# Optimization experiments

Hardware: AMD Instinct MI355X
Metric: run time of the kernel (lower is better)

Reference implementation:

```python
import jax, jax.numpy as jnp
import numpy as np

CUTOFF = 5.0
N_PER_L = (20, 18, 16, 14)   # radial features per angular channel l (max_radial=20, Laplacian-eigenstate style taper)
M_PER_L = (1, 3, 5, 7)       # 2l+1
N_ATOMS = 10000
N_EDGES = 200000
N_SPECIES = 100
PSEUDO = 4

_FREQS = np.concatenate([np.arange(1, nl + 1) for nl in N_PER_L]).astype(np.float32)  # [sum(N_PER_L)]


def _radial(r):
    # r: [P] -> [P, sum(N_PER_L)]. Sine (spherical Laplacian eigenstate style) basis with smooth cosine cutoff.
    rc = jnp.clip(r, 0.0, CUTOFF)
    fc = 0.5 * (jnp.cos(jnp.pi * rc / CUTOFF) + 1.0)            # [P]
    return jnp.sin(jnp.asarray(_FREQS) * (jnp.pi / CUTOFF) * r[:, None]) * fc[:, None]


def _angular(R, r):
    # real spherical harmonics up to l=3, [P, 16], ordered l-major (m = -l..l)
    u = R / (r[:, None] + 1e-12)
    x, y, z = u[:, 0], u[:, 1], u[:, 2]
    x2, y2, z2 = x * x, y * y, z * z
    cols = [
        jnp.full_like(x, 0.28209479177387814),
        0.4886025119029199 * y, 0.4886025119029199 * z, 0.4886025119029199 * x,
        1.0925484305920792 * x * y, 1.0925484305920792 * y * z,
        0.31539156525252005 * (3.0 * z2 - 1.0),
        1.0925484305920792 * x * z, 0.5462742152960396 * (x2 - y2),
        0.5900435899266435 * y * (3.0 * x2 - y2), 2.890611442640554 * x * y * z,
        0.4570457994644658 * y * (5.0 * z2 - 1.0), 0.3731763325901154 * z * (5.0 * z2 - 3.0),
        0.4570457994644658 * x * (5.0 * z2 - 1.0), 1.445305721320277 * z * (x2 - y2),
        0.5900435899266435 * x * (x2 - 3.0 * y2),
    ]
    return jnp.stack(cols, axis=-1)


def setup_inputs() -> dict:
    key = jax.random.key(0)
    k1, k2, k3, k4, k5 = jax.random.split(key, 5)
    return {
        "R_ij": jax.random.normal(k1, (N_EDGES, 3), dtype=jnp.float32) * 1.5,
        "i": jnp.sort(jax.random.randint(k2, (N_EDGES,), 0, N_ATOMS)),
        "j": jax.random.randint(k3, (N_EDGES,), 0, N_ATOMS),
        "species": jax.random.randint(k4, (N_ATOMS,), 0, N_SPECIES),
        "species_embed": jax.random.normal(k5, (N_SPECIES, PSEUDO), dtype=jnp.float32),
    }


def reference(R_ij, i, j, species, species_embed):
    r = jnp.sqrt(jnp.sum(R_ij * R_ij, axis=-1))          # [P]
    radial = _radial(r)                                   # [P, sum n_l]
    angular = _angular(R_ij, r)                           # [P, 16]
    sp = species_embed[species[j]]                        # alchemical species channels, [P, 4]
    outs = []
    off_n = 0
    off_m = 0
    for nl, ml in zip(N_PER_L, M_PER_L):
        rl = radial[:, off_n:off_n + nl]                  # [P, n_l]
        al = angular[:, off_m:off_m + ml]                 # [P, 2l+1]
        e = jnp.einsum('pn,pm,pc->pmnc', rl, al, sp)      # fused outer product per edge
        outs.append(jax.ops.segment_sum(e, i, num_segments=N_ATOMS))  # [n_atoms, 2l+1, n_l, 4]
        off_n += nl
        off_m += ml
    return tuple(outs)
```

## Files before the change

kernel.cpp:

```cpp
#include <hip/hip_runtime.h>

#define N_ATOMS 10000
#define N_EDGES 200000
#define EB 64
#define FEAT 40
#define PI_F 3.14159265358979323846f
#define W_F  0.6283185307179586f

__global__ __launch_bounds__(256) void seg_starts_kernel(
    const int* __restrict__ seg_i, int* __restrict__ starts)
{
    const int a = blockIdx.x * blockDim.x + threadIdx.x;
    if (a > N_ATOMS) return;
    int lo = 0, hi = N_EDGES;
    while (lo < hi) {
        int mid = (lo + hi) >> 1;
        if (seg_i[mid] < a) lo = mid + 1; else hi = mid;
    }
    starts[a] = lo;
}

__global__ __launch_bounds__(128) void sph_expand_kernel(
    const float* __restrict__ R,
    const int*   __restrict__ starts,
    const int*   __restrict__ idx_j,
    const int*   __restrict__ species,
    const float* __restrict__ emb,
    float*       __restrict__ out)
{
    __shared__ float feat[EB][FEAT];
    const int atom = blockIdx.x;
    const int tid  = threadIdx.x;

    int m, np_, nl, offm; long base; int stride;
    {
        int t = tid;
        if (t < 10)      { m = 0;                 np_ = t;          nl = 20; offm = 0; base = 0;        stride = 80;  }
        else if (t < 37) { int q = t - 10; m = q / 9; np_ = q - 9*m; nl = 18; offm = 1; base = 800000;  stride = 216; }
        else if (t < 77) { int q = t - 37; m = q / 8; np_ = q - 8*m; nl = 16; offm = 4; base = 2960000; stride = 320; }
        else             { int q = t - 77; m = q / 7; np_ = q - 7*m; nl = 14; offm = 9; base = 6160000; stride = 392; }
    }
    const int n0   = 2 * np_;
    const int aidx = 20 + offm + m;
    const bool active = (tid < 126);

    float a0x=0.f, a0y=0.f, a0z=0.f, a0w=0.f;
    float a1x=0.f, a1y=0.f, a1z=0.f, a1w=0.f;

    const int start = starts[atom];
    const int end   = starts[atom + 1];

    for (int e0 = start; e0 < end; e0 += EB) {
        const int cnt = min(EB, end - e0);
        __syncthreads();
        if (tid < cnt) {
            const int g = e0 + tid;
            const int jj = idx_j[g];
            const float x = R[3*g + 0];
            const float y = R[3*g + 1];
            const float z = R[3*g + 2];
            const int sidx = species[jj];
            const float r   = sqrtf(x*x + y*y + z*z);
            const float inv = 1.0f / (r + 1e-12f);
            const float ux = x*inv, uy = y*inv, uz = z*inv;
            const float4 spv = *(const float4*)&emb[4 * sidx];

            const float t1 = W_F * r;
            const float s1 = sinf(t1);
            const float c1 = cosf(t1);
            const float fc = (r < 5.0f) ? (0.5f * (c1 + 1.0f)) : 0.0f;
            const float c2x = 2.0f * c1;

            float rb[20];
            {
                float sk_2 = 0.0f, sk_1 = s1;
                rb[0] = s1 * fc;
                #pragma unroll
                for (int k = 1; k < 20; ++k) {
                    const float sk = c2x * sk_1 - sk_2;
                    rb[k] = sk * fc;
                    sk_2 = sk_1; sk_1 = sk;
                }
            }

            const float x2 = ux*ux, y2 = uy*uy, z2 = uz*uz;
            const float c1a = 0.4886025119029199f;
            const float c2a = 1.0925484305920792f;
            float an[16];
            an[0]  = 0.28209479177387814f;
            an[1]  = c1a * uy;
            an[2]  = c1a * uz;
            an[3]  = c1a * ux;
            an[4]  = c2a * ux * uy;
            an[5]  = c2a * uy * uz;
            an[6]  = 0.31539156525252005f * (3.0f*z2 - 1.0f);
            an[7]  = c2a * ux * uz;
            an[8]  = 0.5462742152960396f * (x2 - y2);
            an[9]  = 0.5900435899266435f * uy * (3.0f*x2 - y2);
            an[10] = 2.890611442640554f  * ux * uy * uz;
            an[11] = 0.4570457994644658f * uy * (5.0f*z2 - 1.0f);
            an[12] = 0.3731763325901154f * uz * (5.0f*z2 - 3.0f);
            an[13] = 0.4570457994644658f * ux * (5.0f*z2 - 1.0f);
            an[14] = 1.445305721320277f  * uz * (x2 - y2);
            an[15] = 0.5900435899266435f * ux * (x2 - 3.0f*y2);

            float4* row = (float4*)&feat[tid][0];
            row[0] = float4{rb[0],  rb[1],  rb[2],  rb[3]};
            row[1] = float4{rb[4],  rb[5],  rb[6],  rb[7]};
            row[2] = float4{rb[8],  rb[9],  rb[10], rb[11]};
            row[3] = float4{rb[12], rb[13], rb[14], rb[15]};
            row[4] = float4{rb[16], rb[17], rb[18], rb[19]};
            row[5] = float4{an[0],  an[1],  an[2],  an[3]};
            row[6] = float4{an[4],  an[5],  an[6],  an[7]};
            row[7] = float4{an[8],  an[9],  an[10], an[11]};
            row[8] = float4{an[12], an[13], an[14], an[15]};
            row[9] = spv;
        }
        __syncthreads();
        if (active) {
            for (int s = 0; s < cnt; ++s) {
                const float* f = &feat[s][0];
                const float2 rv  = *(const float2*)(f + n0);
                const float  av  = f[aidx];
                const float4 spv = *(const float4*)(f + 36);
                const float p0 = rv.x * av;
                const float p1 = rv.y * av;
                a0x += p0 * spv.x; a0y += p0 * spv.y; a0z += p0 * spv.z; a0w += p0 * spv.w;
                a1x += p1 * spv.x; a1y += p1 * spv.y; a1z += p1 * spv.z; a1w += p1 * spv.w;
            }
        }
    }

    if (active) {
        const size_t o = (size_t)base + (size_t)atom * (size_t)stride + (size_t)(m * nl + n0) * 4;
        *(float4*)&out[o]     = float4{a0x, a0y, a0z, a0w};
        *(float4*)&out[o + 4] = float4{a1x, a1y, a1z, a1w};
    }
}

extern "C" void kernel_launch(void* const* d_in, const int* in_sizes, int n_in,
                              void* d_out, int out_size, void* d_ws, size_t ws_size,
                              hipStream_t stream) {
    const float* R    = (const float*)d_in[0];
    const int*   i_   = (const int*)  d_in[1];
    const int*   j_   = (const int*)  d_in[2];
    const int*   sp   = (const int*)  d_in[3];
    const float* emb  = (const float*)d_in[4];
    float* out = (float*)d_out;
    int*   starts = (int*)d_ws;

    seg_starts_kernel<<<(N_ATOMS + 256) / 256, 256, 0, stream>>>(i_, starts);
    sph_expand_kernel<<<N_ATOMS, 128, 0, stream>>>(R, starts, j_, sp, emb, out);
}
```

Baseline: 91.46 us.

## Map one atom per wavefront with 4x2 register tiles per lane

After: 97.53 us. +6.6%, slower.

```diff
diff --git a/kernel.cpp b/kernel.cpp
--- a/kernel.cpp
+++ b/kernel.cpp
@@ -3,9 +3,8 @@
 #define N_ATOMS 10000
 #define N_EDGES 200000
 #define EB 64
-#define FEAT 40
-#define PI_F 3.14159265358979323846f
-#define W_F  0.6283185307179586f
+#define FP 52
+#define W_F 0.6283185307179586f
 
 __global__ __launch_bounds__(256) void seg_starts_kernel(
     const int* __restrict__ seg_i, int* __restrict__ starts)
@@ -20,7 +19,7 @@
     starts[a] = lo;
 }
 
-__global__ __launch_bounds__(128) void sph_expand_kernel(
+__global__ __launch_bounds__(256) void sph_expand_kernel(
     const float* __restrict__ R,
     const int*   __restrict__ starts,
     const int*   __restrict__ idx_j,
@@ -28,33 +27,31 @@
     const float* __restrict__ emb,
     float*       __restrict__ out)
 {
-    __shared__ float feat[EB][FEAT];
-    const int atom = blockIdx.x;
-    const int tid  = threadIdx.x;
+    __shared__ float feat[4][EB][FP];
+    const int wave = threadIdx.x >> 6;
+    const int lane = threadIdx.x & 63;
+    const int atom = blockIdx.x * 4 + wave;
+    float (*F)[FP] = feat[wave];
 
-    int m, np_, nl, offm; long base; int stride;
-    {
-        int t = tid;
-        if (t < 10)      { m = 0;                 np_ = t;          nl = 20; offm = 0; base = 0;        stride = 80;  }
-        else if (t < 37) { int q = t - 10; m = q / 9; np_ = q - 9*m; nl = 18; offm = 1; base = 800000;  stride = 216; }
-        else if (t < 77) { int q = t - 37; m = q / 8; np_ = q - 8*m; nl = 16; offm = 4; base = 2960000; stride = 320; }
-        else             { int q = t - 77; m = q / 7; np_ = q - 7*m; nl = 14; offm = 9; base = 6160000; stride = 392; }
-    }
-    const int n0   = 2 * np_;
-    const int aidx = 20 + offm + m;
-    const bool active = (tid < 126);
+    int n0 = 0, m0 = 0, m1 = 0, nl = 0, pidx = 0, stride = 0; long base = 0;
+    const bool active = (lane < 43);
+    if (lane < 5)        { n0 = 4*lane;                                   m0 = 0; m1 = 0;                     nl = 20; pidx = 0;          base = 0;       stride = 80;  }
+    else if (lane < 15)  { int q = lane-5;  int pr = q/5;  n0 = 4*(q%5);  m0 = 2*pr; m1 = (m0+1 < 3) ? m0+1 : 2; nl = 18; pidx = 1 + pr;  base = 800000;  stride = 216; }
+    else if (lane < 27)  { int q = lane-15; int pr = q/4;  n0 = 4*(q%4);  m0 = 2*pr; m1 = (m0+1 < 5) ? m0+1 : 4; nl = 16; pidx = 3 + pr;  base = 2960000; stride = 320; }
+    else if (lane < 43)  { int q = lane-27; int pr = q/4;  n0 = 4*(q%4);  m0 = 2*pr; m1 = (m0+1 < 7) ? m0+1 : 6; nl = 14; pidx = 6 + pr;  base = 6160000; stride = 392; }
 
-    float a0x=0.f, a0y=0.f, a0z=0.f, a0w=0.f;
-    float a1x=0.f, a1y=0.f, a1z=0.f, a1w=0.f;
+    float4 acc[8];
+    #pragma unroll
+    for (int k = 0; k < 8; ++k) acc[k] = float4{0.f, 0.f, 0.f, 0.f};
 
     const int start = starts[atom];
     const int end   = starts[atom + 1];
 
     for (int e0 = start; e0 < end; e0 += EB) {
         const int cnt = min(EB, end - e0);
-        __syncthreads();
-        if (tid < cnt) {
-            const int g = e0 + tid;
+
+        if (lane < cnt) {
+            const int g = e0 + lane;
             const int jj = idx_j[g];
             const float x = R[3*g + 0];
             const float y = R[3*g + 1];
@@ -104,37 +101,55 @@
             an[14] = 1.445305721320277f  * uz * (x2 - y2);
             an[15] = 0.5900435899266435f * ux * (x2 - 3.0f*y2);
 
-            float4* row = (float4*)&feat[tid][0];
+            float4* row = (float4*)&F[lane][0];
             row[0] = float4{rb[0],  rb[1],  rb[2],  rb[3]};
             row[1] = float4{rb[4],  rb[5],  rb[6],  rb[7]};
             row[2] = float4{rb[8],  rb[9],  rb[10], rb[11]};
             row[3] = float4{rb[12], rb[13], rb[14], rb[15]};
             row[4] = float4{rb[16], rb[17], rb[18], rb[19]};
-            row[5] = float4{an[0],  an[1],  an[2],  an[3]};
-            row[6] = float4{an[4],  an[5],  an[6],  an[7]};
-            row[7] = float4{an[8],  an[9],  an[10], an[11]};
-            row[8] = float4{an[12], an[13], an[14], an[15]};
-            row[9] = spv;
+            row[5] = float4{an[0],  an[0],  an[1],  an[2]};
+            row[6] = float4{an[3],  an[3],  an[4],  an[5]};
+            row[7] = float4{an[6],  an[7],  an[8],  an[8]};
+            row[8] = float4{an[9],  an[10], an[11], an[12]};
+            row[9] = float4{an[13], an[14], an[15], an[15]};
+            row[10] = spv;
         }
-        __syncthreads();
+        __builtin_amdgcn_wave_barrier();
         if (active) {
             for (int s = 0; s < cnt; ++s) {
-                const float* f = &feat[s][0];
-                const float2 rv  = *(const float2*)(f + n0);
-                const float  av  = f[aidx];
-                const float4 spv = *(const float4*)(f + 36);
-                const float p0 = rv.x * av;
-                const float p1 = rv.y * av;
-                a0x += p0 * spv.x; a0y += p0 * spv.y; a0z += p0 * spv.z; a0w += p0 * spv.w;
-                a1x += p1 * spv.x; a1y += p1 * spv.y; a1z += p1 * spv.z; a1w += p1 * spv.w;
+                const float* f = &F[s][0];
+                const float4 rq = *(const float4*)(f + n0);
+                const float2 ap = *(const float2*)(f + 20 + 2*pidx);
+                const float4 sv = *(const float4*)(f + 40);
+                const float rr[4] = {rq.x, rq.y, rq.z, rq.w};
+                const float aa[2] = {ap.x, ap.y};
+                #pragma unroll
+                for (int mi = 0; mi < 2; ++mi) {
+                    #pragma unroll
+                    for (int ni = 0; ni < 4; ++ni) {
+                        const float p = rr[ni] * aa[mi];
+                        float4& A = acc[mi*4 + ni];
+                        A.x += p * sv.x; A.y += p * sv.y; A.z += p * sv.z; A.w += p * sv.w;
+                    }
+                }
             }
         }
+        __builtin_amdgcn_wave_barrier();
     }
 
     if (active) {
-        const size_t o = (size_t)base + (size_t)atom * (size_t)stride + (size_t)(m * nl + n0) * 4;
-        *(float4*)&out[o]     = float4{a0x, a0y, a0z, a0w};
-        *(float4*)&out[o + 4] = float4{a1x, a1y, a1z, a1w};
+        float* ob = out + base + (size_t)atom * (size_t)stride;
+        #pragma unroll
+        for (int mi = 0; mi < 2; ++mi) {
+            if (mi == 0 || m1 != m0) {
+                const int m = mi ? m1 : m0;
+                #pragma unroll
+                for (int ni = 0; ni < 4; ++ni) {
+                    const int n = n0 + ni;
+                    if (n < nl) *(float4*)(ob + (size_t)(m*nl + n)*4) = acc[mi*4 + ni];
+                }
+            }
+        }
     }
 }
 
@@ -150,5 +165,5 @@
     int*   starts = (int*)d_ws;
 
     seg_starts_kernel<<<(N_ATOMS + 256) / 256, 256, 0, stream>>>(i_, starts);
-    sph_expand_kernel<<<N_ATOMS, 128, 0, stream>>>(R, starts, j_, sp, emb, out);
+    sph_expand_kernel<<<N_ATOMS / 4, 256, 0, stream>>>(R, starts, j_, sp, emb, out);
 }
```
